# Optimization experiments

Hardware: AMD Instinct MI355X
Metric: run time of the kernel (lower is better)

## Reference

```python
import jax, jax.numpy as jnp
import numpy as np

L, B, H, S, D = 28, 3, 16, 1024, 128
VOCAB = 151936
HIST = 64
BEAM_SIZE = 3
TOP_K = 3


def setup_inputs() -> dict:
    key = jax.random.key(0)
    k1, k2, k3, k4 = jax.random.split(key, 4)
    kv = jax.random.normal(k1, (L, B, H, S, D), dtype=jnp.float32)
    logits = jax.random.normal(k2, (B, VOCAB), dtype=jnp.float32)
    save_id = jax.random.randint(k3, (B, HIST), 0, VOCAB, dtype=jnp.int32)
    repeat_penality = jnp.ones((B, VOCAB), dtype=jnp.float32)
    previous_prob = jax.random.normal(k4, (B, 1), dtype=jnp.float32)
    penality_value = jnp.ones((1,), dtype=jnp.float32)
    return {
        "kv": kv,
        "logits": logits,
        "save_id": save_id,
        "repeat_penality": repeat_penality,
        "previous_prob": previous_prob,
        "penality_value": penality_value,
        "beam_size": BEAM_SIZE,
        "topK": TOP_K,
    }


def reference(kv, logits, save_id, repeat_penality, previous_prob, penality_value, beam_size, topK):
    # log_softmax over penalized logits  [beam, vocab]
    lp = jax.nn.log_softmax(logits * repeat_penality, axis=-1)
    # per-beam top-k (sorted, largest)  [beam, topK]
    top_k_prob, top_k_idx = jax.lax.top_k(lp, topK)
    # combine with running beam log-probs and flatten  [beam*topK]
    current_prob = (top_k_prob + previous_prob).reshape(-1)
    # global top-beam selection over beam*topK candidates
    top_beam_prob, top_beam_idx = jax.lax.top_k(current_prob, beam_size)
    beam_index = top_beam_idx // topK                       # [beam] source beam per survivor
    tokens = top_k_idx.reshape(-1)[top_beam_idx]            # [beam] chosen token ids
    # reorder all per-layer KV caches by surviving beams (the heavy gather)
    kv_out = kv[:, beam_index]                              # [L, beam, H, S, D]
    # reorder + update repeat penalty at chosen tokens
    rp = repeat_penality[beam_index]                        # [beam, vocab]
    rp = rp.at[jnp.arange(beam_size), tokens].multiply(penality_value[0])
    tok_col = tokens[:, None].astype(jnp.int32)             # [beam, 1]
    save_id_out = jnp.concatenate([save_id[beam_index], tok_col], axis=-1)
    max_logits_idx = tok_col[0]                             # [1]
    return (kv_out, tok_col, save_id_out, rp, top_beam_prob[:, None], max_logits_idx)
```

## Files before the change

### kernel.cpp

```cpp
#include <hip/hip_runtime.h>
#include <math.h>

#define NL 28
#define NB 3
#define NH 16
#define NS 1024
#define ND 128
#define VOCAB 151936
#define HIST 64

#define CHUNKS 16
#define CHUNK_LEN (VOCAB / CHUNKS)

#define OFF_TOK  176160768
#define OFF_SAVE 176160771
#define OFF_RP   176160966
#define OFF_PROB 176616774
#define OFF_MAX  176616777

#define WS_BEAM 384
#define WS_TOK  388

__device__ __forceinline__ void ins3(float x, int ix, float v[3], int iv[3]) {
    if (x > v[0] || (x == v[0] && ix < iv[0])) {
        v[2] = v[1]; iv[2] = iv[1];
        v[1] = v[0]; iv[1] = iv[0];
        v[0] = x;    iv[0] = ix;
    } else if (x > v[1] || (x == v[1] && ix < iv[1])) {
        v[2] = v[1]; iv[2] = iv[1];
        v[1] = x;    iv[1] = ix;
    } else if (x > v[2] || (x == v[2] && ix < iv[2])) {
        v[2] = x;    iv[2] = ix;
    }
}

__global__ __launch_bounds__(256) void k1_partial(
    const float* __restrict__ logits, const float* __restrict__ rpen,
    float* __restrict__ wsf, int* __restrict__ wsi) {
    const int b = blockIdx.x / CHUNKS;
    const int c = blockIdx.x % CHUNKS;
    const int base = c * CHUNK_LEN;
    const float* lrow = logits + b * VOCAB;
    const float* prow = rpen + b * VOCAB;

    float m = -INFINITY, l = 0.f;
    float v[3] = {-INFINITY, -INFINITY, -INFINITY};
    int iv[3] = {-1, -1, -1};

    for (int j = threadIdx.x; j < CHUNK_LEN; j += 256) {
        int idx = base + j;
        float x = lrow[idx] * prow[idx];
        if (x > m) { l = l * expf(m - x) + 1.f; m = x; }
        else       { l += expf(x - m); }
        ins3(x, idx, v, iv);
    }

    for (int off = 32; off > 0; off >>= 1) {
        float om = __shfl_down(m, off, 64);
        float ol = __shfl_down(l, off, 64);
        float ov[3]; int oi[3];
#pragma unroll
        for (int k = 0; k < 3; ++k) {
            ov[k] = __shfl_down(v[k], off, 64);
            oi[k] = __shfl_down(iv[k], off, 64);
        }
        float M = fmaxf(m, om);
        l = l * expf(m - M) + ol * expf(om - M);
        m = M;
#pragma unroll
        for (int k = 0; k < 3; ++k) ins3(ov[k], oi[k], v, iv);
    }

    __shared__ float sm[4], sl[4], sv[4][3];
    __shared__ int si[4][3];
    const int lane = threadIdx.x & 63;
    const int wid = threadIdx.x >> 6;
    if (lane == 0) {
        sm[wid] = m; sl[wid] = l;
#pragma unroll
        for (int k = 0; k < 3; ++k) { sv[wid][k] = v[k]; si[wid][k] = iv[k]; }
    }
    __syncthreads();
    if (threadIdx.x == 0) {
        for (int w = 1; w < 4; ++w) {
            float M = fmaxf(m, sm[w]);
            l = l * expf(m - M) + sl[w] * expf(sm[w] - M);
            m = M;
#pragma unroll
            for (int k = 0; k < 3; ++k) ins3(sv[w][k], si[w][k], v, iv);
        }
        const int pbase = (b * CHUNKS + c) * 8;
        wsf[pbase + 0] = m;
        wsf[pbase + 1] = l;
#pragma unroll
        for (int k = 0; k < 3; ++k) {
            wsf[pbase + 2 + k] = v[k];
            wsi[pbase + 5 + k] = iv[k];
        }
    }
}

__global__ __launch_bounds__(256) void k2_select(
    const float* __restrict__ prev, const int* __restrict__ save_id,
    const float* __restrict__ wsf, int* __restrict__ wsi,
    float* __restrict__ out) {
    __shared__ float stopv[9];
    __shared__ int stopi[9];
    __shared__ int sbeam[3], stok[3];
    __shared__ float sprob[3];
    const int t = threadIdx.x;

    if (t < NB) {
        float m = -INFINITY, l = 0.f;
        float v[3] = {-INFINITY, -INFINITY, -INFINITY};
        int iv[3] = {-1, -1, -1};
        for (int c = 0; c < CHUNKS; ++c) {
            const int pbase = (t * CHUNKS + c) * 8;
            float pm = wsf[pbase + 0], pl = wsf[pbase + 1];
            float M = fmaxf(m, pm);
            l = l * expf(m - M) + pl * expf(pm - M);
            m = M;
#pragma unroll
            for (int k = 0; k < 3; ++k) ins3(wsf[pbase + 2 + k], wsi[pbase + 5 + k], v, iv);
        }
        const float lse = m + logf(l);
#pragma unroll
        for (int k = 0; k < 3; ++k) {
            stopv[t * 3 + k] = v[k] - lse;
            stopi[t * 3 + k] = iv[k];
        }
    }
    __syncthreads();
    if (t == 0) {
        float cur[9];
        for (int j = 0; j < 9; ++j) cur[j] = stopv[j] + prev[j / 3];
        bool used[9] = {false, false, false, false, false, false, false, false, false};
        for (int i = 0; i < 3; ++i) {
            int best = 0; float bv = -INFINITY;
            for (int j = 0; j < 9; ++j) {
                if (!used[j] && cur[j] > bv) { bv = cur[j]; best = j; }
            }
            used[best] = true;
            sbeam[i] = best / 3;
            stok[i]  = stopi[best];
            sprob[i] = bv;
        }
        for (int i = 0; i < 3; ++i) {
            wsi[WS_BEAM + i] = sbeam[i];
            wsi[WS_TOK + i]  = stok[i];
        }
    }
    __syncthreads();
    if (t < 3) {
        out[OFF_TOK + t]  = (float)stok[t];
        out[OFF_PROB + t] = sprob[t];
    }
    if (t == 0) out[OFF_MAX] = (float)stok[0];
    if (t < 3 * (HIST + 1)) {
        const int i = t / (HIST + 1);
        const int h = t - i * (HIST + 1);
        out[OFF_SAVE + t] = (h < HIST) ? (float)save_id[sbeam[i] * HIST + h]
                                       : (float)stok[i];
    }
}

__global__ __launch_bounds__(256) void k3_kv(
    const float4* __restrict__ kv, const int* __restrict__ wsi,
    float4* __restrict__ out) {
    __shared__ int sbeam[3];
    if (threadIdx.x < 3) sbeam[threadIdx.x] = wsi[WS_BEAM + threadIdx.x];
    __syncthreads();
    const unsigned PER = (NH * NS * ND) / 4;
    unsigned idx = blockIdx.x * 256u + threadIdx.x;
    unsigned li = idx >> 19;
    unsigned off = idx & (PER - 1);
    unsigned l = li / 3;
    unsigned i = li - l * 3;
    out[idx] = kv[(l * 3 + sbeam[i]) * PER + off];
}

__global__ __launch_bounds__(256) void k4_rp(
    const float* __restrict__ rpen, const float* __restrict__ pen,
    const int* __restrict__ wsi, float* __restrict__ out) {
    int idx = blockIdx.x * 256 + threadIdx.x;
    if (idx >= NB * VOCAB) return;
    int i = idx / VOCAB;
    int v = idx - i * VOCAB;
    float x = rpen[wsi[WS_BEAM + i] * VOCAB + v];
    if (v == wsi[WS_TOK + i]) x *= pen[0];
    out[OFF_RP + idx] = x;
}

extern "C" void kernel_launch(void* const* d_in, const int* in_sizes, int n_in,
                              void* d_out, int out_size, void* d_ws, size_t ws_size,
                              hipStream_t stream) {
    const float* kv      = (const float*)d_in[0];
    const float* logits  = (const float*)d_in[1];
    const int*   save_id = (const int*)d_in[2];
    const float* rpen    = (const float*)d_in[3];
    const float* prev    = (const float*)d_in[4];
    const float* pen     = (const float*)d_in[5];
    float* out = (float*)d_out;
    float* wsf = (float*)d_ws;
    int*   wsi = (int*)d_ws;

    k1_partial<<<NB * CHUNKS, 256, 0, stream>>>(logits, rpen, wsf, wsi);
    k2_select<<<1, 256, 0, stream>>>(prev, save_id, wsf, wsi, out);

    const int kv4 = NL * NB * NH * NS * ND / 4;
    k3_kv<<<kv4 / 256, 256, 0, stream>>>((const float4*)kv, wsi, (float4*)out);

    k4_rp<<<(NB * VOCAB + 255) / 256, 256, 0, stream>>>(rpen, pen, wsi, out);
}
```

Baseline: 1.056 ms.

## Fuse KV gather and penalty reorder into one kernel with nontemporal wide copies

Merges the KV-cache beam gather and the repeat-penalty reorder into a single launch. Each KV block now copies 8 float4 per thread with nontemporal loads and stores, and the source beam is resolved once per block. The vocab reduction is also split into 64 chunks instead of 16 for more parallelism in the first pass, with workspace offsets moved to fit. The aim is to cut launch overhead and get closer to peak bandwidth on the 700 MB copy, at the cost of higher register use per thread.

```diff
diff --git a/kernel.cpp b/kernel.cpp
--- a/kernel.cpp
+++ b/kernel.cpp
@@ -9,7 +9,7 @@
 #define VOCAB 151936
 #define HIST 64
 
-#define CHUNKS 16
+#define CHUNKS 64
 #define CHUNK_LEN (VOCAB / CHUNKS)
 
 #define OFF_TOK  176160768
@@ -18,8 +18,10 @@
 #define OFF_PROB 176616774
 #define OFF_MAX  176616777
 
-#define WS_BEAM 384
-#define WS_TOK  388
+#define WS_BEAM 1536
+#define WS_TOK  1540
+
+typedef float f32x4 __attribute__((ext_vector_type(4)));
 
 __device__ __forceinline__ void ins3(float x, int ix, float v[3], int iv[3]) {
     if (x > v[0] || (x == v[0] && ix < iv[0])) {
@@ -164,31 +166,40 @@
     }
 }
 
-__global__ __launch_bounds__(256) void k3_kv(
-    const float4* __restrict__ kv, const int* __restrict__ wsi,
-    float4* __restrict__ out) {
-    __shared__ int sbeam[3];
-    if (threadIdx.x < 3) sbeam[threadIdx.x] = wsi[WS_BEAM + threadIdx.x];
-    __syncthreads();
-    const unsigned PER = (NH * NS * ND) / 4;
-    unsigned idx = blockIdx.x * 256u + threadIdx.x;
-    unsigned li = idx >> 19;
-    unsigned off = idx & (PER - 1);
-    unsigned l = li / 3;
-    unsigned i = li - l * 3;
-    out[idx] = kv[(l * 3 + sbeam[i]) * PER + off];
-}
-
-__global__ __launch_bounds__(256) void k4_rp(
-    const float* __restrict__ rpen, const float* __restrict__ pen,
-    const int* __restrict__ wsi, float* __restrict__ out) {
-    int idx = blockIdx.x * 256 + threadIdx.x;
-    if (idx >= NB * VOCAB) return;
-    int i = idx / VOCAB;
-    int v = idx - i * VOCAB;
-    float x = rpen[wsi[WS_BEAM + i] * VOCAB + v];
-    if (v == wsi[WS_TOK + i]) x *= pen[0];
-    out[OFF_RP + idx] = x;
+#define PER4      ((NH * NS * ND) / 4)
+#define KV4       (NL * NB * PER4)
+#define KVBLOCKS  (KV4 / 2048)
+#define RPBLOCKS  ((NB * VOCAB + 255) / 256)
+
+__global__ __launch_bounds__(256) void k3_fused(
+    const f32x4* __restrict__ kv, const float* __restrict__ rpen,
+    const float* __restrict__ pen, const int* __restrict__ wsi,
+    f32x4* __restrict__ out4, float* __restrict__ out) {
+    if (blockIdx.x < KVBLOCKS) {
+        const unsigned li = blockIdx.x >> 8;
+        const unsigned l  = li / 3u;
+        const unsigned i  = li - l * 3u;
+        const int sb = wsi[WS_BEAM + i];
+        const unsigned dst = blockIdx.x * 2048u + threadIdx.x;
+        const unsigned src = (l * 3u + (unsigned)sb) * PER4
+                           + (blockIdx.x & 255u) * 2048u + threadIdx.x;
+        f32x4 r[8];
+#pragma unroll
+        for (int k = 0; k < 8; ++k)
+            r[k] = __builtin_nontemporal_load(&kv[src + k * 256u]);
+#pragma unroll
+        for (int k = 0; k < 8; ++k)
+            __builtin_nontemporal_store(r[k], &out4[dst + k * 256u]);
+    } else {
+        const int idx = (blockIdx.x - KVBLOCKS) * 256 + threadIdx.x;
+        if (idx < NB * VOCAB) {
+            const int i = idx / VOCAB;
+            const int v = idx - i * VOCAB;
+            float x = rpen[wsi[WS_BEAM + i] * VOCAB + v];
+            if (v == wsi[WS_TOK + i]) x *= pen[0];
+            out[OFF_RP + idx] = x;
+        }
+    }
 }
 
 extern "C" void kernel_launch(void* const* d_in, const int* in_sizes, int n_in,
@@ -206,9 +217,6 @@
 
     k1_partial<<<NB * CHUNKS, 256, 0, stream>>>(logits, rpen, wsf, wsi);
     k2_select<<<1, 256, 0, stream>>>(prev, save_id, wsf, wsi, out);
-
-    const int kv4 = NL * NB * NH * NS * ND / 4;
-    k3_kv<<<kv4 / 256, 256, 0, stream>>>((const float4*)kv, wsi, (float4*)out);
-
-    k4_rp<<<(NB * VOCAB + 255) / 256, 256, 0, stream>>>(rpen, pen, wsi, out);
-}
+    k3_fused<<<KVBLOCKS + RPBLOCKS, 256, 0, stream>>>(
+        (const f32x4*)kv, rpen, pen, wsi, (f32x4*)out, out);
+}
```

Result: slower. 1.112 ms (+5.3%).
